# Kernel tuning notes

Measured on AMD Instinct MI355X. Metric: run time of the kernel, lower is better.

The kernel has to match this reference:

```python
import jax, jax.numpy as jnp
import numpy as np

DIM = 1024
D_STATE = 16
D_CONV = 4
EXPAND = 2
D_INNER = EXPAND * DIM
BATCH = 4
SEQ = 2048


def setup_inputs() -> dict:
    key = jax.random.key(0)
    ks = jax.random.split(key, 9)
    n = lambda i, shape, scale=0.02: (jax.random.normal(ks[i], shape, jnp.float32) * scale)
    return {
        "x": jax.random.normal(ks[0], (BATCH, SEQ, DIM), jnp.float32),
        "in_proj_w": n(1, (D_INNER, DIM)),
        "conv_w": n(2, (D_INNER, D_CONV), 0.1),          # depthwise kernel (groups=d_inner)
        "x_proj_w": n(3, (2 * D_STATE + 1, D_INNER)),
        "dt_proj_w": n(4, (D_INNER, 1), 1.0),
        "dt_proj_b": n(5, (D_INNER,), 0.1),
        "A_log": jax.random.normal(ks[6], (D_INNER, D_STATE), jnp.float32),
        "D": jnp.ones((D_INNER,), jnp.float32),
        "out_proj_w": n(7, (DIM, D_INNER)),
        "norm_w": jnp.ones((DIM,), jnp.float32),
        "norm_b": jnp.zeros((DIM,), jnp.float32),
    }


def reference(x, in_proj_w, conv_w, x_proj_w, dt_proj_w, dt_proj_b,
              A_log, D, out_proj_w, norm_w, norm_b):
    Bsz, L, _ = x.shape
    shortcut = x

    # LayerNorm
    mu = jnp.mean(x, axis=-1, keepdims=True)
    var = jnp.var(x, axis=-1, keepdims=True)
    h = (x - mu) / jnp.sqrt(var + 1e-5) * norm_w + norm_b

    # in_proj: [B,L,dim] -> [B,L,d_inner]
    h = h @ in_proj_w.T

    # causal depthwise conv1d (padding d_conv-1, truncate to L)
    hp = jnp.pad(h, ((0, 0), (D_CONV - 1, 0), (0, 0)))
    h_conv = sum(hp[:, k:k + L, :] * conv_w[:, k] for k in range(D_CONV))
    h = jax.nn.silu(h_conv)

    # x_proj -> dt (1), B (d_state), C (d_state)
    proj = h @ x_proj_w.T
    dt_in = proj[..., :1]
    B_param = proj[..., 1:1 + D_STATE]      # [B,L,d_state]
    C_param = proj[..., 1 + D_STATE:]       # [B,L,d_state]
    dt = jax.nn.softplus(dt_in @ dt_proj_w.T + dt_proj_b)  # [B,L,d_inner]

    A = -jnp.exp(A_log)                     # [d_inner, d_state]

    def step(state, inp):
        dt_t, B_t, C_t, x_t = inp           # [B,d_inner],[B,ds],[B,ds],[B,d_inner]
        state = jnp.exp(A[None] * dt_t[:, :, None]) * state \
                + B_t[:, None, :] * x_t[:, :, None]          # [B,d_inner,d_state]
        y = jnp.einsum('bnd,bd->bn', state, C_t) + D * x_t   # [B,d_inner]
        return state, y

    init = jnp.zeros((Bsz, D_INNER, D_STATE), x.dtype)
    xs = (jnp.swapaxes(dt, 0, 1), jnp.swapaxes(B_param, 0, 1),
          jnp.swapaxes(C_param, 0, 1), jnp.swapaxes(h, 0, 1))
    state, ys = jax.lax.scan(step, init, xs)
    y = jnp.swapaxes(ys, 0, 1)              # [B,L,d_inner]

    out = jax.nn.silu(y) @ out_proj_w.T + shortcut
    return out, state
```

## Files before the change

kernel.cpp:

```cpp
#include <hip/hip_runtime.h>

typedef unsigned short u16;
typedef unsigned int u32;
typedef __attribute__((ext_vector_type(8))) short short8;
typedef __attribute__((ext_vector_type(4))) float f32x4;
typedef __attribute__((ext_vector_type(2))) float f32x2;
typedef __attribute__((ext_vector_type(8))) unsigned short ushort8_t;

#define SEQ 2048
#define DIM 1024
#define DINNER 2048
#define NPROJ 33
#define NPROJ_PAD 48
#define LC 16
#define NC 128

__device__ __forceinline__ u16 f2bf(float f) {
  union { float f; u32 u; } v; v.f = f;
  u32 r = (v.u + 0x7fffu + ((v.u >> 16) & 1u)) >> 16;
  return (u16)r;
}
__device__ __forceinline__ float bf2f(u16 s) {
  union { u32 u; float f; } v; v.u = ((u32)s) << 16;
  return v.f;
}
__device__ __forceinline__ float lo_bf(u32 w) {
  union { u32 u; float f; } v; v.u = w << 16; return v.f;
}
__device__ __forceinline__ float hi_bf(u32 w) {
  union { u32 u; float f; } v; v.u = w & 0xffff0000u; return v.f;
}
__device__ __forceinline__ float fexp2(float x) {
#if __has_builtin(__builtin_amdgcn_exp2f)
  return __builtin_amdgcn_exp2f(x);
#else
  return __expf(x * 0.69314718f);
#endif
}
__device__ __forceinline__ float frcp(float x) {
#if __has_builtin(__builtin_amdgcn_rcpf)
  return __builtin_amdgcn_rcpf(x);
#else
  return 1.f / x;
#endif
}
__device__ __forceinline__ float softplus(float x) {
  return fmaxf(x, 0.f) + __logf(1.f + __expf(-fabsf(x)));
}
__device__ __forceinline__ f32x2 sp2(float v) { f32x2 r; r.x = v; r.y = v; return r; }
__device__ __forceinline__ f32x2 pkfma(f32x2 a, f32x2 b, f32x2 c) {
  return __builtin_elementwise_fma(a, b, c);
}
__device__ __forceinline__ void async16(const void* g, void* l) {
  __builtin_amdgcn_global_load_lds(
      (const __attribute__((address_space(1))) u32*)g,
      (__attribute__((address_space(3))) u32*)l, 16, 0, 0);
}

__global__ void cast_w_kernel(const float* __restrict__ w1, const float* __restrict__ w3,
                              u16* __restrict__ o1, u16* __restrict__ o3) {
  int i = blockIdx.x * 256 + threadIdx.x;
  float4 a = ((const float4*)w1)[i];
  float4 b = ((const float4*)w3)[i];
  ushort4 oa, ob;
  oa.x = f2bf(a.x); oa.y = f2bf(a.y); oa.z = f2bf(a.z); oa.w = f2bf(a.w);
  ob.x = f2bf(b.x); ob.y = f2bf(b.y); ob.z = f2bf(b.z); ob.w = f2bf(b.w);
  ((ushort4*)o1)[i] = oa;
  ((ushort4*)o3)[i] = ob;
}

__global__ void cast_w2pad_kernel(const float* __restrict__ src, u16* __restrict__ dst) {
  int i = blockIdx.x * 256 + threadIdx.x;
  int j = i >> 11, k = i & 2047;
  dst[i] = (j < NPROJ) ? f2bf(src[j * 2048 + k]) : (u16)0;
}

__global__ __launch_bounds__(256) void ln_kernel(const float* __restrict__ x,
                                                 const float* __restrict__ w,
                                                 const float* __restrict__ b,
                                                 u16* __restrict__ h) {
  const int row = blockIdx.x;
  const int tid = threadIdx.x;
  const int lane = tid & 63, wave = tid >> 6;
  const float4 v = ((const float4*)(x + (size_t)row * DIM))[tid];
  float s = v.x + v.y + v.z + v.w;
  float q = v.x * v.x + v.y * v.y + v.z * v.z + v.w * v.w;
  for (int off = 32; off; off >>= 1) {
    s += __shfl_down(s, off);
    q += __shfl_down(q, off);
  }
  __shared__ float sbuf[8];
  if (lane == 0) { sbuf[wave] = s; sbuf[4 + wave] = q; }
  __syncthreads();
  float tot = sbuf[0] + sbuf[1] + sbuf[2] + sbuf[3];
  float totq = sbuf[4] + sbuf[5] + sbuf[6] + sbuf[7];
  const float mean = tot * (1.0f / DIM);
  const float var = totq * (1.0f / DIM) - mean * mean;
  const float rs = rsqrtf(var + 1e-5f);
  const float4 wv = ((const float4*)w)[tid];
  const float4 bv = ((const float4*)b)[tid];
  ushort4 o;
  o.x = f2bf((v.x - mean) * rs * wv.x + bv.x);
  o.y = f2bf((v.y - mean) * rs * wv.y + bv.y);
  o.z = f2bf((v.z - mean) * rs * wv.z + bv.z);
  o.w = f2bf((v.w - mean) * rs * wv.w + bv.w);
  ((ushort4*)(h + (size_t)row * DIM))[tid] = o;
}

__global__ __launch_bounds__(512) void gemm_bf16_kernel(const u16* __restrict__ A,
                                                        const u16* __restrict__ Bt,
                                                        u16* __restrict__ C,
                                                        int K, int N) {
  __shared__ u16 As[128 * 32];
  __shared__ u16 Bs[128 * 32];
  const int tid = threadIdx.x;
  const int lane = tid & 63, wave = tid >> 6;
  const int wm = wave >> 2, wn = wave & 3;
  const int row16 = lane & 15, quad = lane >> 4;
  const int flat = blockIdx.x + gridDim.x * blockIdx.y;
  const int xcd = flat & 7;
  const int sidx = flat >> 3;
  const int bm = xcd * 8 + (sidx & 7);
  const int bn = sidx >> 3;
  f32x4 acc[4][2] = {};
  const u16* Ablk = A + (size_t)bm * 128 * K;
  const u16* Bblk = Bt + (size_t)bn * 128 * K;
  const int r = tid >> 2, cc = (tid & 3) * 8;
  for (int k0 = 0; k0 < K; k0 += 32) {
    async16(Ablk + (size_t)r * K + k0 + cc, &As[tid * 8]);
    async16(Bblk + (size_t)r * K + k0 + cc, &Bs[tid * 8]);
    __syncthreads();
    short8 af[4], bfr[2];
#pragma unroll
    for (int i = 0; i < 4; ++i)
      af[i] = *(const short8*)&As[(wm * 64 + i * 16 + row16) * 32 + quad * 8];
#pragma unroll
    for (int j = 0; j < 2; ++j)
      bfr[j] = *(const short8*)&Bs[(wn * 32 + j * 16 + row16) * 32 + quad * 8];
#pragma unroll
    for (int i = 0; i < 4; ++i)
#pragma unroll
      for (int j = 0; j < 2; ++j)
        acc[i][j] = __builtin_amdgcn_mfma_f32_16x16x32_bf16(af[i], bfr[j], acc[i][j], 0, 0, 0);
    __syncthreads();
  }
#pragma unroll
  for (int i = 0; i < 4; ++i) {
    int m = bm * 128 + wm * 64 + i * 16 + quad * 4;
#pragma unroll
    for (int j = 0; j < 2; ++j) {
      int n = bn * 128 + wn * 32 + j * 16 + row16;
#pragma unroll
      for (int rr = 0; rr < 4; ++rr)
        C[(size_t)(m + rr) * N + n] = f2bf(acc[i][j][rr]);
    }
  }
}

__global__ __launch_bounds__(512) void gemm_out_kernel(const u16* __restrict__ A,
                                                       const u16* __restrict__ Bt,
                                                       const float* __restrict__ resid,
                                                       float* __restrict__ C,
                                                       int K, int N) {
  __shared__ u16 As[128 * 32];
  __shared__ u16 Bs[128 * 32];
  const int tid = threadIdx.x;
  const int lane = tid & 63, wave = tid >> 6;
  const int wm = wave >> 2, wn = wave & 3;
  const int row16 = lane & 15, quad = lane >> 4;
  const int flat = blockIdx.x + gridDim.x * blockIdx.y;
  const int xcd = flat & 7;
  const int sidx = flat >> 3;
  const int bm = xcd * 8 + (sidx & 7);
  const int bn = sidx >> 3;
  f32x4 acc[4][2] = {};
  const u16* Ablk = A + (size_t)bm * 128 * K;
  const u16* Bblk = Bt + (size_t)bn * 128 * K;
  const int r = tid >> 2, cc = (tid & 3) * 8;
  for (int k0 = 0; k0 < K; k0 += 32) {
    async16(Ablk + (size_t)r * K + k0 + cc, &As[tid * 8]);
    async16(Bblk + (size_t)r * K + k0 + cc, &Bs[tid * 8]);
    __syncthreads();
    short8 af[4], bfr[2];
#pragma unroll
    for (int i = 0; i < 4; ++i)
      af[i] = *(const short8*)&As[(wm * 64 + i * 16 + row16) * 32 + quad * 8];
#pragma unroll
    for (int j = 0; j < 2; ++j)
      bfr[j] = *(const short8*)&Bs[(wn * 32 + j * 16 + row16) * 32 + quad * 8];
#pragma unroll
    for (int i = 0; i < 4; ++i)
#pragma unroll
      for (int j = 0; j < 2; ++j)
        acc[i][j] = __builtin_amdgcn_mfma_f32_16x16x32_bf16(af[i], bfr[j], acc[i][j], 0, 0, 0);
    __syncthreads();
  }
#pragma unroll
  for (int i = 0; i < 4; ++i) {
    int m = bm * 128 + wm * 64 + i * 16 + quad * 4;
#pragma unroll
    for (int j = 0; j < 2; ++j) {
      int n = bn * 128 + wn * 32 + j * 16 + row16;
#pragma unroll
      for (int rr = 0; rr < 4; ++rr) {
        size_t idx = (size_t)(m + rr) * N + n;
        C[idx] = acc[i][j][rr] + resid[idx];
      }
    }
  }
}

__global__ __launch_bounds__(256) void conv_silu_kernel(const u16* __restrict__ c1,
                                                        const float* __restrict__ cw,
                                                        u16* __restrict__ cs) {
  const int tid = threadIdx.x;
  const int dg = tid * 8;
  const size_t m0 = (size_t)blockIdx.x * 8;
  const int l0 = (int)(m0 & (SEQ - 1));
  float w[4][8];
  {
    const float4* cw4 = (const float4*)(cw + (size_t)dg * 4);
#pragma unroll
    for (int c = 0; c < 8; ++c) {
      float4 v = cw4[c];
      w[0][c] = v.x; w[1][c] = v.y; w[2][c] = v.z; w[3][c] = v.w;
    }
  }
  const u16* base = c1 + m0 * DINNER + dg;
  ushort8_t win0, win1, win2, win3;
  const ushort8_t zero = (ushort8_t)0;
  if (l0 == 0) {
    win0 = zero; win1 = zero; win2 = zero;
  } else {
    win0 = *(const ushort8_t*)(base - 3 * DINNER);
    win1 = *(const ushort8_t*)(base - 2 * DINNER);
    win2 = *(const ushort8_t*)(base - 1 * DINNER);
  }
  win3 = *(const ushort8_t*)(base);
#pragma unroll
  for (int t = 0; t < 8; ++t) {
    ushort8_t nxt = win3;
    if (t < 7) nxt = *(const ushort8_t*)(base + (size_t)(t + 1) * DINNER);
    ushort8_t o;
#pragma unroll
    for (int c = 0; c < 8; ++c) {
      float acc = bf2f((u16)win0[c]) * w[0][c];
      acc = fmaf(bf2f((u16)win1[c]), w[1][c], acc);
      acc = fmaf(bf2f((u16)win2[c]), w[2][c], acc);
      acc = fmaf(bf2f((u16)win3[c]), w[3][c], acc);
      const float s = acc * frcp(1.f + __expf(-acc));
      o[c] = (unsigned short)f2bf(s);
    }
    *(ushort8_t*)(cs + (m0 + t) * DINNER + dg) = o;
    win0 = win1; win1 = win2; win2 = win3; win3 = nxt;
  }
}

__global__ __launch_bounds__(128) void gemm_w2_kernel(const u16* __restrict__ A,
                                                      const u16* __restrict__ Bt,
                                                      float* __restrict__ C) {
  __shared__ u16 As[32 * 32];
  __shared__ u16 Bs[48 * 32];
  const int tid = threadIdx.x;
  const int lane = tid & 63, wave = tid >> 6;
  const int row16 = lane & 15, quad = lane >> 4;
  const int bm = blockIdx.x;
  const int K = DINNER;
  f32x4 acc[3] = {};
  const u16* Ablk = A + (size_t)bm * 32 * K;
  const int r = tid >> 2, cc = (tid & 3) * 8;
  for (int k0 = 0; k0 < K; k0 += 32) {
    async16(Ablk + (size_t)r * K + k0 + cc, &As[tid * 8]);
    async16(Bt + (size_t)r * K + k0 + cc, &Bs[tid * 8]);
    if (tid < 64)
      async16(Bt + (size_t)(32 + r) * K + k0 + cc, &Bs[1024 + tid * 8]);
    __syncthreads();
    short8 af = *(const short8*)&As[(wave * 16 + row16) * 32 + quad * 8];
    short8 bfr[3];
#pragma unroll
    for (int j = 0; j < 3; ++j)
      bfr[j] = *(const short8*)&Bs[(j * 16 + row16) * 32 + quad * 8];
#pragma unroll
    for (int j = 0; j < 3; ++j)
      acc[j] = __builtin_amdgcn_mfma_f32_16x16x32_bf16(af, bfr[j], acc[j], 0, 0, 0);
    __syncthreads();
  }
  const int m = bm * 32 + wave * 16 + quad * 4;
#pragma unroll
  for (int j = 0; j < 3; ++j) {
    const int n = j * 16 + row16;
#pragma unroll
    for (int rr = 0; rr < 4; ++rr)
      C[(size_t)(m + rr) * NPROJ_PAD + n] = acc[j][rr];
  }
}


__global__ __launch_bounds__(128) void scan_phase1(const float* __restrict__ proj,
                                                   const u16* __restrict__ xs,
                                                   const float* __restrict__ dtw_,
                                                   const float* __restrict__ dtb_,
                                                   const float* __restrict__ A_log,
                                                   u16* __restrict__ S,
                                                   float* __restrict__ Tdt) {
  __shared__ float Bsh[LC][16];
  __shared__ float DTin[LC];
  const int tid = threadIdx.x;
  const int d0 = blockIdx.x * 256 + tid * 2;
  const int c = blockIdx.y;
  const int b = blockIdx.z;
  const size_t mrow = (size_t)b * SEQ + c * LC;
  for (int i = tid; i < LC * 16; i += 128) {
    int t = i >> 4, n = i & 15;
    Bsh[t][n] = proj[(mrow + t) * NPROJ_PAD + 1 + n];
  }
  if (tid < LC) DTin[tid] = proj[(mrow + tid) * NPROJ_PAD];
  __syncthreads();
  f32x2 An2[16];
#pragma unroll
  for (int n = 0; n < 16; ++n) {
    An2[n].x = -__expf(A_log[(size_t)d0 * 16 + n]) * 1.44269504f;
    An2[n].y = -__expf(A_log[(size_t)(d0 + 1) * 16 + n]) * 1.44269504f;
  }
  const float2 dtwv = *(const float2*)(dtw_ + d0);
  const float2 dtbv = *(const float2*)(dtb_ + d0);
  f32x2 dtw2; dtw2.x = dtwv.x; dtw2.y = dtwv.y;
  f32x2 dtb2; dtb2.x = dtbv.x; dtb2.y = dtbv.y;
  f32x2 s[16];
#pragma unroll
  for (int n = 0; n < 16; ++n) s[n] = sp2(0.f);
  f32x2 Tsum = sp2(0.f);
  const u16* xp = xs + mrow * DINNER + d0;
  u32 xw = *(const u32*)xp;
#pragma unroll 2
  for (int t = 0; t < LC; ++t) {
    f32x2 xv; xv.x = lo_bf(xw); xv.y = hi_bf(xw);
    if (t + 1 < LC) xw = *(const u32*)(xp + (size_t)(t + 1) * DINNER);
    f32x2 dtv = pkfma(sp2(DTin[t]), dtw2, dtb2);
    f32x2 sp; sp.x = softplus(dtv.x); sp.y = softplus(dtv.y);
    Tsum += sp;
    const float4* Br = (const float4*)&Bsh[t][0];
#pragma unroll
    for (int q = 0; q < 4; ++q) {
      const float4 Bq = Br[q];
      const float bqa[4] = {Bq.x, Bq.y, Bq.z, Bq.w};
#pragma unroll
      for (int j = 0; j < 4; ++j) {
        const int n = q * 4 + j;
        f32x2 e = An2[n] * sp;
        f32x2 dk; dk.x = fexp2(e.x); dk.y = fexp2(e.y);
        s[n] = pkfma(dk, s[n], sp2(bqa[j]) * xv);
      }
    }
  }
  const size_t so = ((size_t)(b * NC + c) * DINNER + d0) * 16;
  ushort8_t o0, o1, o2, o3;
#pragma unroll
  for (int j = 0; j < 8; ++j) {
    o0[j] = f2bf(s[j].x);     o1[j] = f2bf(s[8 + j].x);
    o2[j] = f2bf(s[j].y);     o3[j] = f2bf(s[8 + j].y);
  }
  *(ushort8_t*)(S + so) = o0;       *(ushort8_t*)(S + so + 8) = o1;
  *(ushort8_t*)(S + so + 16) = o2;  *(ushort8_t*)(S + so + 24) = o3;
  *(float2*)(Tdt + (size_t)(b * NC + c) * DINNER + d0) = make_float2(Tsum.x, Tsum.y);
}

__global__ __launch_bounds__(256) void scan_phase2(const float* __restrict__ A_log,
                                                   u16* __restrict__ S,
                                                   const float* __restrict__ Tdt,
                                                   float* __restrict__ out_state) {
  const int idx = blockIdx.x * 256 + threadIdx.x;
  const int n = idx & 15;
  const int d = (idx >> 4) & (DINNER - 1);
  const int b = idx >> 15;
  const float An = -__expf(A_log[d * 16 + n]) * 1.44269504f;
  float prev = 0.f;
#pragma unroll 4
  for (int c = 0; c < NC; ++c) {
    const size_t base = (size_t)(b * NC + c) * DINNER + d;
    const float T = Tdt[base];
    const size_t so = base * 16 + n;
    const float loc = bf2f(S[so]);
    S[so] = f2bf(prev);
    prev = fmaf(fexp2(An * T), prev, loc);
  }
  out_state[((size_t)b * DINNER + d) * 16 + n] = prev;
}

__global__ __launch_bounds__(128) void scan_phase3(const float* __restrict__ proj,
                                                   const u16* __restrict__ xs,
                                                   const float* __restrict__ dtw_,
                                                   const float* __restrict__ dtb_,
                                                   const float* __restrict__ A_log,
                                                   const float* __restrict__ Dp,
                                                   const u16* __restrict__ S,
                                                   u16* __restrict__ ysil) {
  __shared__ float Bsh[LC][16];
  __shared__ float Csh[LC][16];
  __shared__ float DTin[LC];
  const int tid = threadIdx.x;
  const int d0 = blockIdx.x * 256 + tid * 2;
  const int c = blockIdx.y;
  const int b = blockIdx.z;
  const size_t mrow = (size_t)b * SEQ + c * LC;
  for (int i = tid; i < LC * 16; i += 128) {
    int t = i >> 4, n = i & 15;
    Bsh[t][n] = proj[(mrow + t) * NPROJ_PAD + 1 + n];
    Csh[t][n] = proj[(mrow + t) * NPROJ_PAD + 17 + n];
  }
  if (tid < LC) DTin[tid] = proj[(mrow + tid) * NPROJ_PAD];
  __syncthreads();
  f32x2 An2[16];
#pragma unroll
  for (int n = 0; n < 16; ++n) {
    An2[n].x = -__expf(A_log[(size_t)d0 * 16 + n]) * 1.44269504f;
    An2[n].y = -__expf(A_log[(size_t)(d0 + 1) * 16 + n]) * 1.44269504f;
  }
  const float2 dtwv = *(const float2*)(dtw_ + d0);
  const float2 dtbv = *(const float2*)(dtb_ + d0);
  const float2 Ddv = *(const float2*)(Dp + d0);
  f32x2 dtw2; dtw2.x = dtwv.x; dtw2.y = dtwv.y;
  f32x2 dtb2; dtb2.x = dtbv.x; dtb2.y = dtbv.y;
  f32x2 Dd2; Dd2.x = Ddv.x; Dd2.y = Ddv.y;
  f32x2 s[16];
  const size_t so = ((size_t)(b * NC + c) * DINNER + d0) * 16;
  {
    ushort8_t v0 = *(const ushort8_t*)(S + so);
    ushort8_t v1 = *(const ushort8_t*)(S + so + 8);
    ushort8_t v2 = *(const ushort8_t*)(S + so + 16);
    ushort8_t v3 = *(const ushort8_t*)(S + so + 24);
#pragma unroll
    for (int j = 0; j < 8; ++j) {
      s[j].x = bf2f((u16)v0[j]);     s[8 + j].x = bf2f((u16)v1[j]);
      s[j].y = bf2f((u16)v2[j]);     s[8 + j].y = bf2f((u16)v3[j]);
    }
  }
  const u16* xp = xs + mrow * DINNER + d0;
  u16* yp = ysil + mrow * DINNER + d0;
  u32 xw = *(const u32*)xp;
#pragma unroll 2
  for (int t = 0; t < LC; ++t) {
    f32x2 xv; xv.x = lo_bf(xw); xv.y = hi_bf(xw);
    if (t + 1 < LC) xw = *(const u32*)(xp + (size_t)(t + 1) * DINNER);
    f32x2 dtv = pkfma(sp2(DTin[t]), dtw2, dtb2);
    f32x2 sp; sp.x = softplus(dtv.x); sp.y = softplus(dtv.y);
    f32x2 y = Dd2 * xv;
    const float4* Br = (const float4*)&Bsh[t][0];
    const float4* Cr = (const float4*)&Csh[t][0];
#pragma unroll
    for (int q = 0; q < 4; ++q) {
      const float4 Bq = Br[q];
      const float4 Cq = Cr[q];
      const float bqa[4] = {Bq.x, Bq.y, Bq.z, Bq.w};
      const float cqa[4] = {Cq.x, Cq.y, Cq.z, Cq.w};
#pragma unroll
      for (int j = 0; j < 4; ++j) {
        const int n = q * 4 + j;
        f32x2 e = An2[n] * sp;
        f32x2 dk; dk.x = fexp2(e.x); dk.y = fexp2(e.y);
        s[n] = pkfma(dk, s[n], sp2(bqa[j]) * xv);
        y = pkfma(sp2(cqa[j]), s[n], y);
      }
    }
    const float sy0 = y.x * frcp(1.f + __expf(-y.x));
    const float sy1 = y.y * frcp(1.f + __expf(-y.y));
    const u32 ow = (u32)f2bf(sy0) | ((u32)f2bf(sy1) << 16);
    *(u32*)(yp + (size_t)t * DINNER) = ow;
  }
}

extern "C" void kernel_launch(void* const* d_in, const int* in_sizes, int n_in,
                              void* d_out, int out_size, void* d_ws, size_t ws_size,
                              hipStream_t stream) {
  const float* x = (const float*)d_in[0];
  const float* in_proj_w = (const float*)d_in[1];
  const float* conv_w = (const float*)d_in[2];
  const float* x_proj_w = (const float*)d_in[3];
  const float* dt_proj_w = (const float*)d_in[4];
  const float* dt_proj_b = (const float*)d_in[5];
  const float* A_log = (const float*)d_in[6];
  const float* Dvec = (const float*)d_in[7];
  const float* out_proj_w = (const float*)d_in[8];
  const float* norm_w = (const float*)d_in[9];
  const float* norm_b = (const float*)d_in[10];

  char* ws = (char*)d_ws;
  u16* h = (u16*)(ws + 0);
  u16* w1b = (u16*)(ws + 16777216);
  u16* w3b = (u16*)(ws + 20971520);
  u16* w2b = (u16*)(ws + 25165824);
  u16* c1 = (u16*)(ws + 25362432);
  u16* ysil = c1;
  u16* cs = (u16*)(ws + 58916864);
  float* proj = (float*)(ws + 92471296);
  float* Tdt = (float*)(ws + 94044160);

  float* out = (float*)d_out;
  float* out_state = out + (size_t)4 * SEQ * DIM;
  u16* Sbuf = (u16*)d_out;

  cast_w_kernel<<<2048, 256, 0, stream>>>(in_proj_w, out_proj_w, w1b, w3b);
  cast_w2pad_kernel<<<384, 256, 0, stream>>>(x_proj_w, w2b);
  ln_kernel<<<8192, 256, 0, stream>>>(x, norm_w, norm_b, h);
  gemm_bf16_kernel<<<dim3(DINNER / 128, 64), 512, 0, stream>>>(h, w1b, c1, DIM, DINNER);
  conv_silu_kernel<<<1024, 256, 0, stream>>>(c1, conv_w, cs);
  gemm_w2_kernel<<<256, 128, 0, stream>>>(cs, w2b, proj);
  scan_phase1<<<dim3(DINNER / 256, NC, 4), 128, 0, stream>>>(proj, cs, dt_proj_w, dt_proj_b,
                                                             A_log, Sbuf, Tdt);
  scan_phase2<<<512, 256, 0, stream>>>(A_log, Sbuf, Tdt, out_state);
  scan_phase3<<<dim3(DINNER / 256, NC, 4), 128, 0, stream>>>(proj, cs, dt_proj_w, dt_proj_b,
                                                             A_log, Dvec, Sbuf, ysil);
  gemm_out_kernel<<<dim3(DIM / 128, 64), 512, 0, stream>>>(ysil, w3b, x, out, DINNER, DIM);
}
```

Measured before the change: 366.7 us.

## Precompute folded A table, read B/C/dt directly from proj, widen scan blocks

Adds a kernel that computes -exp(A_log)*log2e once into an interleaved table, so the scan phases load it with float4 instead of recomputing exp per block. The x_proj weight rows are permuted so B and C start at offset 0 and 16, letting the scan kernels read B/C/dt straight from global memory (uniform, cacheable loads) rather than staging them through shared memory with a barrier. Scan blocks grow from 128 to 256 threads, halving the grid. The cost is more uniform global loads in the inner loop and one extra small launch.

```diff
diff --git a/kernel.cpp b/kernel.cpp
--- a/kernel.cpp
+++ b/kernel.cpp
@@ -72,7 +72,18 @@
 __global__ void cast_w2pad_kernel(const float* __restrict__ src, u16* __restrict__ dst) {
   int i = blockIdx.x * 256 + threadIdx.x;
   int j = i >> 11, k = i & 2047;
-  dst[i] = (j < NPROJ) ? f2bf(src[j * 2048 + k]) : (u16)0;
+  u16 v;
+  if (j < 32) v = f2bf(src[(1 + j) * 2048 + k]);
+  else if (j == 32) v = f2bf(src[k]);
+  else v = (u16)0;
+  dst[i] = v;
+}
+
+__global__ void foldA_kernel(const float* __restrict__ A_log, float* __restrict__ A2) {
+  int i = blockIdx.x * 256 + threadIdx.x;
+  int p = i >> 5, n2 = i & 31;
+  int d = p * 2 + (n2 & 1), n = n2 >> 1;
+  A2[i] = -__expf(A_log[d * 16 + n]) * 1.44269504f;
 }
 
 __global__ __launch_bounds__(256) void ln_kernel(const float* __restrict__ x,
@@ -296,31 +307,27 @@
 }
 
 
-__global__ __launch_bounds__(128) void scan_phase1(const float* __restrict__ proj,
+__global__ __launch_bounds__(256) void scan_phase1(const float* __restrict__ proj,
                                                    const u16* __restrict__ xs,
                                                    const float* __restrict__ dtw_,
                                                    const float* __restrict__ dtb_,
-                                                   const float* __restrict__ A_log,
+                                                   const float* __restrict__ A2,
                                                    u16* __restrict__ S,
                                                    float* __restrict__ Tdt) {
-  __shared__ float Bsh[LC][16];
-  __shared__ float DTin[LC];
-  const int tid = threadIdx.x;
-  const int d0 = blockIdx.x * 256 + tid * 2;
+  const int tid = threadIdx.x;
+  const int d0 = blockIdx.x * 512 + tid * 2;
   const int c = blockIdx.y;
   const int b = blockIdx.z;
   const size_t mrow = (size_t)b * SEQ + c * LC;
-  for (int i = tid; i < LC * 16; i += 128) {
-    int t = i >> 4, n = i & 15;
-    Bsh[t][n] = proj[(mrow + t) * NPROJ_PAD + 1 + n];
-  }
-  if (tid < LC) DTin[tid] = proj[(mrow + tid) * NPROJ_PAD];
-  __syncthreads();
   f32x2 An2[16];
-#pragma unroll
-  for (int n = 0; n < 16; ++n) {
-    An2[n].x = -__expf(A_log[(size_t)d0 * 16 + n]) * 1.44269504f;
-    An2[n].y = -__expf(A_log[(size_t)(d0 + 1) * 16 + n]) * 1.44269504f;
+  {
+    const float4* Ap = (const float4*)(A2 + (size_t)(d0 >> 1) * 32);
+#pragma unroll
+    for (int q = 0; q < 8; ++q) {
+      float4 v = Ap[q];
+      An2[2 * q].x = v.x;     An2[2 * q].y = v.y;
+      An2[2 * q + 1].x = v.z; An2[2 * q + 1].y = v.w;
+    }
   }
   const float2 dtwv = *(const float2*)(dtw_ + d0);
   const float2 dtbv = *(const float2*)(dtb_ + d0);
@@ -330,16 +337,18 @@
 #pragma unroll
   for (int n = 0; n < 16; ++n) s[n] = sp2(0.f);
   f32x2 Tsum = sp2(0.f);
+  const float* pr = proj + mrow * NPROJ_PAD;
   const u16* xp = xs + mrow * DINNER + d0;
   u32 xw = *(const u32*)xp;
 #pragma unroll 2
   for (int t = 0; t < LC; ++t) {
     f32x2 xv; xv.x = lo_bf(xw); xv.y = hi_bf(xw);
     if (t + 1 < LC) xw = *(const u32*)(xp + (size_t)(t + 1) * DINNER);
-    f32x2 dtv = pkfma(sp2(DTin[t]), dtw2, dtb2);
+    const float dtin = pr[32];
+    f32x2 dtv = pkfma(sp2(dtin), dtw2, dtb2);
     f32x2 sp; sp.x = softplus(dtv.x); sp.y = softplus(dtv.y);
     Tsum += sp;
-    const float4* Br = (const float4*)&Bsh[t][0];
+    const float4* Br = (const float4*)pr;
 #pragma unroll
     for (int q = 0; q < 4; ++q) {
       const float4 Bq = Br[q];
@@ -352,6 +361,7 @@
         s[n] = pkfma(dk, s[n], sp2(bqa[j]) * xv);
       }
     }
+    pr += NPROJ_PAD;
   }
   const size_t so = ((size_t)(b * NC + c) * DINNER + d0) * 16;
   ushort8_t o0, o1, o2, o3;
@@ -365,7 +375,7 @@
   *(float2*)(Tdt + (size_t)(b * NC + c) * DINNER + d0) = make_float2(Tsum.x, Tsum.y);
 }
 
-__global__ __launch_bounds__(256) void scan_phase2(const float* __restrict__ A_log,
+__global__ __launch_bounds__(256) void scan_phase2(const float* __restrict__ A2,
                                                    u16* __restrict__ S,
                                                    const float* __restrict__ Tdt,
                                                    float* __restrict__ out_state) {
@@ -373,7 +383,7 @@
   const int n = idx & 15;
   const int d = (idx >> 4) & (DINNER - 1);
   const int b = idx >> 15;
-  const float An = -__expf(A_log[d * 16 + n]) * 1.44269504f;
+  const float An = A2[((d >> 1) << 5) + (n << 1) + (d & 1)];
   float prev = 0.f;
 #pragma unroll 4
   for (int c = 0; c < NC; ++c) {
@@ -387,34 +397,28 @@
   out_state[((size_t)b * DINNER + d) * 16 + n] = prev;
 }
 
-__global__ __launch_bounds__(128) void scan_phase3(const float* __restrict__ proj,
+__global__ __launch_bounds__(256) void scan_phase3(const float* __restrict__ proj,
                                                    const u16* __restrict__ xs,
                                                    const float* __restrict__ dtw_,
                                                    const float* __restrict__ dtb_,
-                                                   const float* __restrict__ A_log,
+                                                   const float* __restrict__ A2,
                                                    const float* __restrict__ Dp,
                                                    const u16* __restrict__ S,
                                                    u16* __restrict__ ysil) {
-  __shared__ float Bsh[LC][16];
-  __shared__ float Csh[LC][16];
-  __shared__ float DTin[LC];
-  const int tid = threadIdx.x;
-  const int d0 = blockIdx.x * 256 + tid * 2;
+  const int tid = threadIdx.x;
+  const int d0 = blockIdx.x * 512 + tid * 2;
   const int c = blockIdx.y;
   const int b = blockIdx.z;
   const size_t mrow = (size_t)b * SEQ + c * LC;
-  for (int i = tid; i < LC * 16; i += 128) {
-    int t = i >> 4, n = i & 15;
-    Bsh[t][n] = proj[(mrow + t) * NPROJ_PAD + 1 + n];
-    Csh[t][n] = proj[(mrow + t) * NPROJ_PAD + 17 + n];
-  }
-  if (tid < LC) DTin[tid] = proj[(mrow + tid) * NPROJ_PAD];
-  __syncthreads();
   f32x2 An2[16];
-#pragma unroll
-  for (int n = 0; n < 16; ++n) {
-    An2[n].x = -__expf(A_log[(size_t)d0 * 16 + n]) * 1.44269504f;
-    An2[n].y = -__expf(A_log[(size_t)(d0 + 1) * 16 + n]) * 1.44269504f;
+  {
+    const float4* Ap = (const float4*)(A2 + (size_t)(d0 >> 1) * 32);
+#pragma unroll
+    for (int q = 0; q < 8; ++q) {
+      float4 v = Ap[q];
+      An2[2 * q].x = v.x;     An2[2 * q].y = v.y;
+      An2[2 * q + 1].x = v.z; An2[2 * q + 1].y = v.w;
+    }
   }
   const float2 dtwv = *(const float2*)(dtw_ + d0);
   const float2 dtbv = *(const float2*)(dtb_ + d0);
@@ -435,6 +439,7 @@
       s[j].y = bf2f((u16)v2[j]);     s[8 + j].y = bf2f((u16)v3[j]);
     }
   }
+  const float* pr = proj + mrow * NPROJ_PAD;
   const u16* xp = xs + mrow * DINNER + d0;
   u16* yp = ysil + mrow * DINNER + d0;
   u32 xw = *(const u32*)xp;
@@ -442,11 +447,12 @@
   for (int t = 0; t < LC; ++t) {
     f32x2 xv; xv.x = lo_bf(xw); xv.y = hi_bf(xw);
     if (t + 1 < LC) xw = *(const u32*)(xp + (size_t)(t + 1) * DINNER);
-    f32x2 dtv = pkfma(sp2(DTin[t]), dtw2, dtb2);
+    const float dtin = pr[32];
+    f32x2 dtv = pkfma(sp2(dtin), dtw2, dtb2);
     f32x2 sp; sp.x = softplus(dtv.x); sp.y = softplus(dtv.y);
     f32x2 y = Dd2 * xv;
-    const float4* Br = (const float4*)&Bsh[t][0];
-    const float4* Cr = (const float4*)&Csh[t][0];
+    const float4* Br = (const float4*)pr;
+    const float4* Cr = (const float4*)(pr + 16);
 #pragma unroll
     for (int q = 0; q < 4; ++q) {
       const float4 Bq = Br[q];
@@ -466,6 +472,7 @@
     const float sy1 = y.y * frcp(1.f + __expf(-y.y));
     const u32 ow = (u32)f2bf(sy0) | ((u32)f2bf(sy1) << 16);
     *(u32*)(yp + (size_t)t * DINNER) = ow;
+    pr += NPROJ_PAD;
   }
 }
 
@@ -494,6 +501,7 @@
   u16* cs = (u16*)(ws + 58916864);
   float* proj = (float*)(ws + 92471296);
   float* Tdt = (float*)(ws + 94044160);
+  float* A2 = (float*)(ws + 98238464);
 
   float* out = (float*)d_out;
   float* out_state = out + (size_t)4 * SEQ * DIM;
@@ -501,14 +509,15 @@
 
   cast_w_kernel<<<2048, 256, 0, stream>>>(in_proj_w, out_proj_w, w1b, w3b);
   cast_w2pad_kernel<<<384, 256, 0, stream>>>(x_proj_w, w2b);
+  foldA_kernel<<<128, 256, 0, stream>>>(A_log, A2);
   ln_kernel<<<8192, 256, 0, stream>>>(x, norm_w, norm_b, h);
   gemm_bf16_kernel<<<dim3(DINNER / 128, 64), 512, 0, stream>>>(h, w1b, c1, DIM, DINNER);
   conv_silu_kernel<<<1024, 256, 0, stream>>>(c1, conv_w, cs);
   gemm_w2_kernel<<<256, 128, 0, stream>>>(cs, w2b, proj);
-  scan_phase1<<<dim3(DINNER / 256, NC, 4), 128, 0, stream>>>(proj, cs, dt_proj_w, dt_proj_b,
-                                                             A_log, Sbuf, Tdt);
-  scan_phase2<<<512, 256, 0, stream>>>(A_log, Sbuf, Tdt, out_state);
-  scan_phase3<<<dim3(DINNER / 256, NC, 4), 128, 0, stream>>>(proj, cs, dt_proj_w, dt_proj_b,
-                                                             A_log, Dvec, Sbuf, ysil);
+  scan_phase1<<<dim3(DINNER / 512, NC, 4), 256, 0, stream>>>(proj, cs, dt_proj_w, dt_proj_b,
+                                                             A2, Sbuf, Tdt);
+  scan_phase2<<<512, 256, 0, stream>>>(A2, Sbuf, Tdt, out_state);
+  scan_phase3<<<dim3(DINNER / 512, NC, 4), 256, 0, stream>>>(proj, cs, dt_proj_w, dt_proj_b,
+                                                             A2, Dvec, Sbuf, ysil);
   gemm_out_kernel<<<dim3(DIM / 128, 64), 512, 0, stream>>>(ysil, w3b, x, out, DINNER, DIM);
 }
```

New measurement: 369.4 us. Within noise of the previous version (+0.7%).
